# Optimization experiments

Hardware: AMD Instinct MI355X
Metric: run time of the kernel (lower is better)

Reference implementation:

```python
import jax, jax.numpy as jnp
import numpy as np
import math

B, T, D, H = 2, 2048, 1024, 16
HD = D // H


def setup_inputs() -> dict:
    key = jax.random.key(0)
    k1, k2, k3 = jax.random.split(key, 3)
    x = jax.random.normal(k1, (B, T, D), dtype=jnp.float32)
    attn_mask = jnp.ones((B, T), dtype=jnp.int32)
    W_qkv = jax.random.normal(k2, (D, 3 * D), dtype=jnp.float32) * (1.0 / math.sqrt(D))
    W_out = jax.random.normal(k3, (D, D), dtype=jnp.float32) * (1.0 / math.sqrt(D))
    return {"x": x, "attn_mask": attn_mask, "W_qkv": W_qkv, "W_out": W_out}


def reference(x, attn_mask, W_qkv, W_out):
    Bx, Tx, Dx = x.shape
    qkv = jnp.einsum("btd,de->bte", x, W_qkv)  # (B,T,3D)
    q, k, v = jnp.split(qkv, 3, axis=-1)
    # (B,T,D) -> (B,H,T,hd)
    q = q.reshape(Bx, Tx, H, HD).transpose(0, 2, 1, 3)
    k = k.reshape(Bx, Tx, H, HD).transpose(0, 2, 1, 3)
    v = v.reshape(Bx, Tx, H, HD).transpose(0, 2, 1, 3)
    scale = 1.0 / math.sqrt(HD)
    scores = jnp.einsum("bhqd,bhkd->bhqk", q, k) * scale  # (B,H,T,T)
    # padding mask over keys: (B,T) -> (B,1,1,T)
    mask = attn_mask[:, None, None, :]
    scores = jnp.where(mask == 0, jnp.float32(-jnp.inf), scores)
    attn = jax.nn.softmax(scores, axis=-1)
    out = jnp.einsum("bhqk,bhkd->bhqd", attn, v)  # (B,H,T,hd)
    out = out.transpose(0, 2, 1, 3).reshape(Bx, Tx, Dx)
    return jnp.einsum("btd,de->bte", out, W_out)
```

## Files before the change

kernel.cpp:

```cpp
#include <hip/hip_runtime.h>

#define B_ 2
#define T_ 2048
#define D_ 1024
#define H_ 16
#define HD_ 64
#define NT_ (B_*T_)

typedef __attribute__((ext_vector_type(8))) short bf16x8;
typedef __attribute__((ext_vector_type(4))) float f32x4;
typedef __attribute__((ext_vector_type(16))) float f32x16;
typedef __attribute__((ext_vector_type(4))) int i32x4;

#define MFMA32(a, b, c) __builtin_amdgcn_mfma_f32_32x32x16_bf16((a), (b), (c), 0, 0, 0)

static __device__ __forceinline__ unsigned short f2bf(float f) {
    union { float f; unsigned u; } v; v.f = f;
    unsigned r = v.u + 0x7fffu + ((v.u >> 16) & 1u);
    return (unsigned short)(r >> 16);
}

static __device__ __forceinline__ float exp2a(float x) {
    float r; asm("v_exp_f32 %0, %1" : "=v"(r) : "v"(x)); return r;
}

static __device__ __forceinline__ unsigned cvt_pk_bf16(float lo, float hi) {
    unsigned r; asm("v_cvt_pk_bf16_f32 %0, %1, %2" : "=v"(r) : "v"(lo), "v"(hi)); return r;
}

static __device__ __forceinline__ void gload_lds16(const unsigned short* g, unsigned short* l) {
    __builtin_amdgcn_global_load_lds(
        (const __attribute__((address_space(1))) unsigned int*)g,
        (__attribute__((address_space(3))) unsigned int*)l, 16, 0, 0);
}

static __device__ __forceinline__ void xcd_swz(int& bx, int& by) {
    int gx = gridDim.x, nwg = gx * gridDim.y;
    int flat = by * gx + bx;
    int cpx = nwg >> 3;
    int swz = (flat & 7) * cpx + (flat >> 3);
    bx = swz % gx; by = swz / gx;
}

__global__ __launch_bounds__(256) void prep_all(
    const float* __restrict__ x, unsigned short* __restrict__ Xb,
    const float* __restrict__ Wqkv, unsigned short* __restrict__ WqkvT,
    const float* __restrict__ Wout, unsigned short* __restrict__ WoutT) {
    __shared__ float tile[32][33];
    int bid = blockIdx.x, tid = threadIdx.x;
    if (bid < 2048) {
        int base = (bid * 256 + tid) * 8;
        f32x4 a = *(const f32x4*)(x + base);
        f32x4 b = *(const f32x4*)(x + base + 4);
        unsigned short o[8];
#pragma unroll
        for (int j = 0; j < 4; ++j) { o[j] = f2bf(a[j]); o[j + 4] = f2bf(b[j]); }
        *(i32x4*)(Xb + base) = *(const i32x4*)o;
        return;
    }
    const float* in; unsigned short* out; int R, C, bx, by;
    if (bid < 5120) {
        int tb = bid - 2048; bx = tb % 96; by = tb / 96;
        in = Wqkv; out = WqkvT; R = 1024; C = 3072;
    } else {
        int tb = bid - 5120; bx = tb & 31; by = tb >> 5;
        in = Wout; out = WoutT; R = 1024; C = 1024;
    }
    int tx = tid & 31, ty = tid >> 5;
    int c0 = bx * 32, r0 = by * 32;
#pragma unroll
    for (int j = 0; j < 32; j += 8)
        tile[ty + j][tx] = in[(size_t)(r0 + ty + j) * C + c0 + tx];
    __syncthreads();
#pragma unroll
    for (int j = 0; j < 32; j += 8)
        out[(size_t)(c0 + ty + j) * R + r0 + tx] = f2bf(tile[tx][ty + j]);
}

template <int EPI>
__global__ __launch_bounds__(256) void gemm_bt(
    const unsigned short* __restrict__ A, const unsigned short* __restrict__ Bt,
    float* __restrict__ C,
    unsigned short* __restrict__ Qo, unsigned short* __restrict__ Ko,
    unsigned short* __restrict__ Vo,
    int M, int N, int K) {
    __shared__ __align__(16) unsigned short As[128 * 64];
    __shared__ __align__(16) unsigned short Bs[128 * 64];
    int tid = threadIdx.x;
    int wv = tid >> 6, lane = tid & 63;
    int wr = wv >> 1, wc = wv & 1;
    int l15 = lane & 15, lg = lane >> 4;
    int bx = blockIdx.x, by = blockIdx.y;
    xcd_swz(bx, by);
    int tm = by * 128, tn = bx * 128;
    f32x4 acc[4][4] = {};

    int lrow = lane >> 3;
    int scol = ((lane & 7) ^ (lrow & 7)) * 8;
    int rsw = l15 & 7;

    for (int kt = 0; kt < K; kt += 64) {
        __syncthreads();
#pragma unroll
        for (int c = 0; c < 4; ++c) {
            int chunk = wv + c * 4;
            gload_lds16(A + (size_t)(tm + chunk * 8 + lrow) * K + kt + scol, As + chunk * 512);
            gload_lds16(Bt + (size_t)(tn + chunk * 8 + lrow) * K + kt + scol, Bs + chunk * 512);
        }
        __syncthreads();
#pragma unroll
        for (int kk = 0; kk < 2; ++kk) {
            bf16x8 af[4], bfr[4];
#pragma unroll
            for (int m = 0; m < 4; ++m) {
                int row = wr * 64 + m * 16 + l15;
                af[m] = *(const bf16x8*)(As + row * 64 + (((kk * 4 + lg) ^ rsw) * 8));
            }
#pragma unroll
            for (int n = 0; n < 4; ++n) {
                int row = wc * 64 + n * 16 + l15;
                bfr[n] = *(const bf16x8*)(Bs + row * 64 + (((kk * 4 + lg) ^ rsw) * 8));
            }
#pragma unroll
            for (int m = 0; m < 4; ++m)
#pragma unroll
                for (int n = 0; n < 4; ++n)
                    acc[m][n] = __builtin_amdgcn_mfma_f32_16x16x32_bf16(af[m], bfr[n], acc[m][n], 0, 0, 0);
        }
    }

    if (EPI == 0) {
#pragma unroll
        for (int m = 0; m < 4; ++m) {
            int row0 = tm + wr * 64 + m * 16 + lg * 4;
#pragma unroll
            for (int n = 0; n < 4; ++n) {
                int col = tn + wc * 64 + n * 16 + l15;
#pragma unroll
                for (int r = 0; r < 4; ++r)
                    C[(size_t)(row0 + r) * N + col] = acc[m][n][r];
            }
        }
    } else {
        const float SC = 0.125f * 1.44269504f;
#pragma unroll
        for (int m = 0; m < 4; ++m) {
            int row0 = tm + wr * 64 + m * 16 + lg * 4;
#pragma unroll
            for (int n = 0; n < 4; ++n) {
                int e = tn + wc * 64 + n * 16 + l15;
                int sec = e >> 10, rem = e & 1023;
                int h = rem >> 6, hd = rem & 63;
                int tok = row0;
                int b = tok >> 11, tl = tok & 2047;
                if (sec == 2) {
                    size_t idx0 = ((size_t)(b * H_ + h) * HD_ + hd) * T_ + tl;
                    *(unsigned*)(Vo + idx0)     = cvt_pk_bf16(acc[m][n][0], acc[m][n][1]);
                    *(unsigned*)(Vo + idx0 + 2) = cvt_pk_bf16(acc[m][n][2], acc[m][n][3]);
                } else {
                    unsigned short* dst = (sec == 0) ? Qo : Ko;
                    float sc = (sec == 0) ? SC : 1.0f;
#pragma unroll
                    for (int r = 0; r < 4; ++r)
                        dst[(((size_t)(b * H_ + h) * T_ + tl + r) << 6) + hd] =
                            f2bf(acc[m][n][r] * sc);
                }
            }
        }
    }
}

__global__ __launch_bounds__(256) void gemm_n64(
    const unsigned short* __restrict__ A, const unsigned short* __restrict__ Bt,
    float* __restrict__ C, int M, int N, int K) {
    __shared__ __align__(16) unsigned short As[128 * 64];
    __shared__ __align__(16) unsigned short Bs[64 * 64];
    int tid = threadIdx.x;
    int wv = tid >> 6, lane = tid & 63;
    int wr = wv >> 1, wc = wv & 1;
    int l15 = lane & 15, lg = lane >> 4;
    int bx = blockIdx.x, by = blockIdx.y;
    xcd_swz(bx, by);
    int tm = by * 128, tn = bx * 64;
    f32x4 acc[4][2] = {};

    int lrow = lane >> 3;
    int scol = ((lane & 7) ^ (lrow & 7)) * 8;
    int rsw = l15 & 7;

    for (int kt = 0; kt < K; kt += 64) {
        __syncthreads();
#pragma unroll
        for (int c = 0; c < 4; ++c) {
            int chunk = wv + c * 4;
            gload_lds16(A + (size_t)(tm + chunk * 8 + lrow) * K + kt + scol, As + chunk * 512);
        }
#pragma unroll
        for (int c = 0; c < 2; ++c) {
            int chunk = wv + c * 4;
            gload_lds16(Bt + (size_t)(tn + chunk * 8 + lrow) * K + kt + scol, Bs + chunk * 512);
        }
        __syncthreads();
#pragma unroll
        for (int kk = 0; kk < 2; ++kk) {
            bf16x8 af[4], bfr[2];
#pragma unroll
            for (int m = 0; m < 4; ++m) {
                int row = wr * 64 + m * 16 + l15;
                af[m] = *(const bf16x8*)(As + row * 64 + (((kk * 4 + lg) ^ rsw) * 8));
            }
#pragma unroll
            for (int n = 0; n < 2; ++n) {
                int row = wc * 32 + n * 16 + l15;
                bfr[n] = *(const bf16x8*)(Bs + row * 64 + (((kk * 4 + lg) ^ rsw) * 8));
            }
#pragma unroll
            for (int m = 0; m < 4; ++m)
#pragma unroll
                for (int n = 0; n < 2; ++n)
                    acc[m][n] = __builtin_amdgcn_mfma_f32_16x16x32_bf16(af[m], bfr[n], acc[m][n], 0, 0, 0);
        }
    }

#pragma unroll
    for (int m = 0; m < 4; ++m) {
        int row0 = tm + wr * 64 + m * 16 + lg * 4;
#pragma unroll
        for (int n = 0; n < 2; ++n) {
            int col = tn + wc * 32 + n * 16 + l15;
#pragma unroll
            for (int r = 0; r < 4; ++r)
                C[(size_t)(row0 + r) * N + col] = acc[m][n][r];
        }
    }
}

#define KPAD 72
#define VPAD 136

#define EXCH(PV, HF, FRAG)                                                     \
  do {                                                                         \
    unsigned uA0 = cvt_pk_bf16(PV[8 * HF + 0], PV[8 * HF + 1]);                \
    unsigned uA1 = cvt_pk_bf16(PV[8 * HF + 2], PV[8 * HF + 3]);                \
    unsigned uB0 = cvt_pk_bf16(PV[8 * HF + 4], PV[8 * HF + 5]);                \
    unsigned uB1 = cvt_pk_bf16(PV[8 * HF + 6], PV[8 * HF + 7]);                \
    unsigned snd0 = hi ? uA0 : uB0, snd1 = hi ? uA1 : uB1;                     \
    unsigned rc0 = (unsigned)__shfl_xor((int)snd0, 32);                        \
    unsigned rc1 = (unsigned)__shfl_xor((int)snd1, 32);                        \
    union { bf16x8 v; unsigned u[4]; } Fx;                                     \
    Fx.u[0] = hi ? rc0 : uA0;                                                  \
    Fx.u[1] = hi ? rc1 : uA1;                                                  \
    Fx.u[2] = hi ? uB0 : rc0;                                                  \
    Fx.u[3] = hi ? uB1 : rc1;                                                  \
    FRAG = Fx.v;                                                               \
  } while (0)

__global__ __launch_bounds__(256) void flash_attn(
    const unsigned short* __restrict__ Qg, const unsigned short* __restrict__ Kg,
    const unsigned short* __restrict__ VTg, const int* __restrict__ mask,
    unsigned short* __restrict__ AO) {
    __shared__ __align__(16) unsigned short Ks[128 * KPAD];
    __shared__ __align__(16) unsigned short VTs[64 * VPAD];
    __shared__ float biasS[128];

    int tid = threadIdx.x, wv = tid >> 6, lane = tid & 63;
    int l31 = lane & 31, hi = lane >> 5;
    int bx = blockIdx.x, by = blockIdx.y;
    xcd_swz(bx, by);
    int bh = by;
    int b = bh >> 4, h = bh & 15;
    int q0 = bx * 128;
    const unsigned short* Qb  = Qg  + (size_t)bh * T_ * HD_;
    const unsigned short* Kb  = Kg  + (size_t)bh * T_ * HD_;
    const unsigned short* VTb = VTg + (size_t)bh * HD_ * T_;

    bf16x8 qf[4];
    {
        const unsigned short* qrow = Qb + (size_t)(q0 + wv * 32 + l31) * HD_;
#pragma unroll
        for (int c = 0; c < 4; ++c)
            qf[c] = *(const bf16x8*)(qrow + c * 16 + hi * 8);
    }

    float lp0 = 0.f, lp1 = 0.f, lp2 = 0.f, lp3 = 0.f;
    f32x16 o0 = {}, o1 = {};

    i32x4 kv[4], vvv[4];
#pragma unroll
    for (int c = 0; c < 4; ++c) {
        int idx = tid + c * 256;
        kv[c]  = *(const i32x4*)(Kb + (size_t)(idx >> 3) * HD_ + (idx & 7) * 8);
        vvv[c] = *(const i32x4*)(VTb + (size_t)(idx >> 4) * T_ + (idx & 15) * 8);
    }
    int mA = mask[b * T_ + lane];
    int mB = mask[b * T_ + 64 + lane];

    for (int kt = 0; kt < T_; kt += 128) {
        bool nomask = __all(mA != 0 && mB != 0);
        __syncthreads();
#pragma unroll
        for (int c = 0; c < 4; ++c) {
            int idx = tid + c * 256;
            *(i32x4*)(Ks + (idx >> 3) * KPAD + (idx & 7) * 8) = kv[c];
            *(i32x4*)(VTs + (idx >> 4) * VPAD + (idx & 15) * 8) = vvv[c];
        }
        if (!nomask && wv == 0) {
            biasS[lane]      = mA ? 0.f : -1e30f;
            biasS[64 + lane] = mB ? 0.f : -1e30f;
        }
        if (kt + 128 < T_) {
#pragma unroll
            for (int c = 0; c < 4; ++c) {
                int idx = tid + c * 256;
                kv[c]  = *(const i32x4*)(Kb + (size_t)(kt + 128 + (idx >> 3)) * HD_ + (idx & 7) * 8);
                vvv[c] = *(const i32x4*)(VTb + (size_t)(idx >> 4) * T_ + kt + 128 + (idx & 15) * 8);
            }
            mA = mask[b * T_ + kt + 128 + lane];
            mB = mask[b * T_ + kt + 192 + lane];
        }
        __syncthreads();

#pragma unroll
        for (int hp = 0; hp < 2; ++hp) {
            f32x16 s0 = {}, s1 = {};
            __builtin_amdgcn_s_setprio(1);
#pragma unroll
            for (int c = 0; c < 4; ++c) {
                bf16x8 ka = *(const bf16x8*)(Ks + ((hp * 2 + 0) * 32 + l31) * KPAD + c * 16 + hi * 8);
                s0 = MFMA32(ka, qf[c], s0);
            }
#pragma unroll
            for (int c = 0; c < 4; ++c) {
                bf16x8 kb2 = *(const bf16x8*)(Ks + ((hp * 2 + 1) * 32 + l31) * KPAD + c * 16 + hi * 8);
                s1 = MFMA32(kb2, qf[c], s1);
            }
            __builtin_amdgcn_s_setprio(0);

            if (!nomask) {
#pragma unroll
                for (int i = 0; i < 16; ++i) {
                    int krow = (i & 3) + 8 * (i >> 2) + 4 * hi;
                    s0[i] += biasS[hp * 64 + krow];
                    s1[i] += biasS[hp * 64 + 32 + krow];
                }
            }
#pragma unroll
            for (int i = 0; i < 16; i += 4) {
                s0[i] = exp2a(s0[i]);     s0[i+1] = exp2a(s0[i+1]);
                s0[i+2] = exp2a(s0[i+2]); s0[i+3] = exp2a(s0[i+3]);
                s1[i] = exp2a(s1[i]);     s1[i+1] = exp2a(s1[i+1]);
                s1[i+2] = exp2a(s1[i+2]); s1[i+3] = exp2a(s1[i+3]);
                lp0 += s0[i]   + s1[i];
                lp1 += s0[i+1] + s1[i+1];
                lp2 += s0[i+2] + s1[i+2];
                lp3 += s0[i+3] + s1[i+3];
            }
            bf16x8 fr0, fr1, fr2, fr3;
            EXCH(s0, 0, fr0);
            EXCH(s0, 1, fr1);
            EXCH(s1, 0, fr2);
            EXCH(s1, 1, fr3);

            __builtin_amdgcn_s_setprio(1);
#pragma unroll
            for (int kc = 0; kc < 4; ++kc) {
                bf16x8 fr = (kc == 0) ? fr0 : (kc == 1) ? fr1 : (kc == 2) ? fr2 : fr3;
                bf16x8 va = *(const bf16x8*)(VTs + l31 * VPAD + hp * 64 + kc * 16 + hi * 8);
                bf16x8 vb = *(const bf16x8*)(VTs + (32 + l31) * VPAD + hp * 64 + kc * 16 + hi * 8);
                o0 = MFMA32(fr, va, o0);
                o1 = MFMA32(fr, vb, o1);
            }
            __builtin_amdgcn_s_setprio(0);
        }
    }

    float l_part = (lp0 + lp1) + (lp2 + lp3);
    l_part += __shfl_xor(l_part, 32);

    size_t rowD = (size_t)(b * T_ + q0 + wv * 32) * D_ + h * 64;
#pragma unroll
    for (int i = 0; i < 16; ++i) {
        int qrow = (i & 3) + 8 * (i >> 2) + 4 * hi;
        float lq = __shfl(l_part, qrow);
        float inv = 1.0f / lq;
        AO[rowD + (size_t)qrow * D_ + l31]      = f2bf(o0[i] * inv);
        AO[rowD + (size_t)qrow * D_ + 32 + l31] = f2bf(o1[i] * inv);
    }
}

extern "C" void kernel_launch(void* const* d_in, const int* in_sizes, int n_in,
                              void* d_out, int out_size, void* d_ws, size_t ws_size,
                              hipStream_t stream) {
    const float* x    = (const float*)d_in[0];
    const int*   mask = (const int*)d_in[1];
    const float* Wqkv = (const float*)d_in[2];
    const float* Wout = (const float*)d_in[3];
    float* out = (float*)d_out;
    char* ws = (char*)d_ws;

    unsigned short* Xb    = (unsigned short*)(ws);
    unsigned short* WqkvT = (unsigned short*)(ws + (size_t)(8u << 20));
    unsigned short* WoutT = (unsigned short*)(ws + (size_t)(14u << 20));
    unsigned short* Qg    = (unsigned short*)(ws + (size_t)(16u << 20));
    unsigned short* Kg    = (unsigned short*)(ws + (size_t)(24u << 20));
    unsigned short* VT    = (unsigned short*)(ws + (size_t)(32u << 20));
    unsigned short* AO    = Xb;

    prep_all<<<6144, 256, 0, stream>>>(x, Xb, Wqkv, WqkvT, Wout, WoutT);
    gemm_bt<1><<<dim3(3072 / 128, 4096 / 128), 256, 0, stream>>>(
        Xb, WqkvT, nullptr, Qg, Kg, VT, NT_, 3 * D_, D_);
    flash_attn<<<dim3(T_ / 128, B_ * H_), 256, 0, stream>>>(Qg, Kg, VT, mask, AO);
    gemm_n64<<<dim3(1024 / 64, 4096 / 128), 256, 0, stream>>>(
        AO, WoutT, out, NT_, D_, D_);
}
```

Before: 127.7 us.

## Load K/V fragments directly from global memory, dropping LDS staging and barriers

The flash attention kernel no longer stages K and V^T tiles through shared memory with register prefetch and two __syncthreads per tile. Each wave now loads its MFMA K and V fragments straight from global memory (relying on L2/cache reuse across the 4 waves), and reads the mask directly for the bias. This removes LDS writes and reads and block barriers, but every wave re-fetches the same K/V data from global memory and the loads are no longer software-prefetched, so latency is exposed.

```diff
diff --git a/kernel.cpp b/kernel.cpp
--- a/kernel.cpp
+++ b/kernel.cpp
@@ -235,9 +235,6 @@
     }
 }
 
-#define KPAD 72
-#define VPAD 136
-
 #define EXCH(PV, HF, FRAG)                                                     \
   do {                                                                         \
     unsigned uA0 = cvt_pk_bf16(PV[8 * HF + 0], PV[8 * HF + 1]);                \
@@ -259,10 +256,6 @@
     const unsigned short* __restrict__ Qg, const unsigned short* __restrict__ Kg,
     const unsigned short* __restrict__ VTg, const int* __restrict__ mask,
     unsigned short* __restrict__ AO) {
-    __shared__ __align__(16) unsigned short Ks[128 * KPAD];
-    __shared__ __align__(16) unsigned short VTs[64 * VPAD];
-    __shared__ float biasS[128];
-
     int tid = threadIdx.x, wv = tid >> 6, lane = tid & 63;
     int l31 = lane & 31, hi = lane >> 5;
     int bx = blockIdx.x, by = blockIdx.y;
@@ -285,63 +278,45 @@
     float lp0 = 0.f, lp1 = 0.f, lp2 = 0.f, lp3 = 0.f;
     f32x16 o0 = {}, o1 = {};
 
-    i32x4 kv[4], vvv[4];
-#pragma unroll
-    for (int c = 0; c < 4; ++c) {
-        int idx = tid + c * 256;
-        kv[c]  = *(const i32x4*)(Kb + (size_t)(idx >> 3) * HD_ + (idx & 7) * 8);
-        vvv[c] = *(const i32x4*)(VTb + (size_t)(idx >> 4) * T_ + (idx & 15) * 8);
-    }
-    int mA = mask[b * T_ + lane];
-    int mB = mask[b * T_ + 64 + lane];
+    const unsigned short* VT0 = VTb + (size_t)l31 * T_;
+    const unsigned short* VT1 = VTb + (size_t)(32 + l31) * T_;
 
     for (int kt = 0; kt < T_; kt += 128) {
+        int mA = mask[b * T_ + kt + lane];
+        int mB = mask[b * T_ + kt + 64 + lane];
         bool nomask = __all(mA != 0 && mB != 0);
-        __syncthreads();
-#pragma unroll
-        for (int c = 0; c < 4; ++c) {
-            int idx = tid + c * 256;
-            *(i32x4*)(Ks + (idx >> 3) * KPAD + (idx & 7) * 8) = kv[c];
-            *(i32x4*)(VTs + (idx >> 4) * VPAD + (idx & 15) * 8) = vvv[c];
-        }
-        if (!nomask && wv == 0) {
-            biasS[lane]      = mA ? 0.f : -1e30f;
-            biasS[64 + lane] = mB ? 0.f : -1e30f;
-        }
-        if (kt + 128 < T_) {
+
+#pragma unroll
+        for (int hp = 0; hp < 2; ++hp) {
+            int kbase = kt + hp * 64;
+            const unsigned short* Kr0 = Kb + (size_t)(kbase + l31) * HD_ + hi * 8;
+            const unsigned short* Kr1 = Kb + (size_t)(kbase + 32 + l31) * HD_ + hi * 8;
+            bf16x8 ka[4], kb2[4], va[4], vb[4];
 #pragma unroll
             for (int c = 0; c < 4; ++c) {
-                int idx = tid + c * 256;
-                kv[c]  = *(const i32x4*)(Kb + (size_t)(kt + 128 + (idx >> 3)) * HD_ + (idx & 7) * 8);
-                vvv[c] = *(const i32x4*)(VTb + (size_t)(idx >> 4) * T_ + kt + 128 + (idx & 15) * 8);
-            }
-            mA = mask[b * T_ + kt + 128 + lane];
-            mB = mask[b * T_ + kt + 192 + lane];
-        }
-        __syncthreads();
-
-#pragma unroll
-        for (int hp = 0; hp < 2; ++hp) {
+                ka[c]  = *(const bf16x8*)(Kr0 + c * 16);
+                kb2[c] = *(const bf16x8*)(Kr1 + c * 16);
+            }
+#pragma unroll
+            for (int kc = 0; kc < 4; ++kc) {
+                va[kc] = *(const bf16x8*)(VT0 + kbase + kc * 16 + hi * 8);
+                vb[kc] = *(const bf16x8*)(VT1 + kbase + kc * 16 + hi * 8);
+            }
+
             f32x16 s0 = {}, s1 = {};
             __builtin_amdgcn_s_setprio(1);
 #pragma unroll
-            for (int c = 0; c < 4; ++c) {
-                bf16x8 ka = *(const bf16x8*)(Ks + ((hp * 2 + 0) * 32 + l31) * KPAD + c * 16 + hi * 8);
-                s0 = MFMA32(ka, qf[c], s0);
-            }
-#pragma unroll
-            for (int c = 0; c < 4; ++c) {
-                bf16x8 kb2 = *(const bf16x8*)(Ks + ((hp * 2 + 1) * 32 + l31) * KPAD + c * 16 + hi * 8);
-                s1 = MFMA32(kb2, qf[c], s1);
-            }
+            for (int c = 0; c < 4; ++c) s0 = MFMA32(ka[c], qf[c], s0);
+#pragma unroll
+            for (int c = 0; c < 4; ++c) s1 = MFMA32(kb2[c], qf[c], s1);
             __builtin_amdgcn_s_setprio(0);
 
             if (!nomask) {
 #pragma unroll
                 for (int i = 0; i < 16; ++i) {
                     int krow = (i & 3) + 8 * (i >> 2) + 4 * hi;
-                    s0[i] += biasS[hp * 64 + krow];
-                    s1[i] += biasS[hp * 64 + 32 + krow];
+                    s0[i] += (mask[b * T_ + kbase + krow] != 0) ? 0.f : -1e30f;
+                    s1[i] += (mask[b * T_ + kbase + 32 + krow] != 0) ? 0.f : -1e30f;
                 }
             }
 #pragma unroll
@@ -365,10 +340,8 @@
 #pragma unroll
             for (int kc = 0; kc < 4; ++kc) {
                 bf16x8 fr = (kc == 0) ? fr0 : (kc == 1) ? fr1 : (kc == 2) ? fr2 : fr3;
-                bf16x8 va = *(const bf16x8*)(VTs + l31 * VPAD + hp * 64 + kc * 16 + hi * 8);
-                bf16x8 vb = *(const bf16x8*)(VTs + (32 + l31) * VPAD + hp * 64 + kc * 16 + hi * 8);
-                o0 = MFMA32(fr, va, o0);
-                o1 = MFMA32(fr, vb, o1);
+                o0 = MFMA32(fr, va[kc], o0);
+                o1 = MFMA32(fr, vb[kc], o1);
             }
             __builtin_amdgcn_s_setprio(0);
         }
```

New measurement: 194.0 us. 52.0% more time.

## Fuse fp32-to-bf16 conversion of x into QKV GEMM operand loading

Applied to the files above, without the earlier changes.

Removes the separate pass that converts x to bf16 in the prep kernel. The QKV GEMM now loads fp32 x into registers one k-tile ahead, converts it to bf16 and writes it into swizzled LDS. This cuts a full read and write of the activation tensor and shrinks the prep launch. In exchange the GEMM reads twice as many bytes for A and replaces the async global-to-LDS load with register-staged stores, which adds register pressure.

```diff
diff --git a/kernel.cpp b/kernel.cpp
--- a/kernel.cpp
+++ b/kernel.cpp
@@ -43,27 +43,16 @@
 }
 
 __global__ __launch_bounds__(256) void prep_all(
-    const float* __restrict__ x, unsigned short* __restrict__ Xb,
     const float* __restrict__ Wqkv, unsigned short* __restrict__ WqkvT,
     const float* __restrict__ Wout, unsigned short* __restrict__ WoutT) {
     __shared__ float tile[32][33];
     int bid = blockIdx.x, tid = threadIdx.x;
-    if (bid < 2048) {
-        int base = (bid * 256 + tid) * 8;
-        f32x4 a = *(const f32x4*)(x + base);
-        f32x4 b = *(const f32x4*)(x + base + 4);
-        unsigned short o[8];
-#pragma unroll
-        for (int j = 0; j < 4; ++j) { o[j] = f2bf(a[j]); o[j + 4] = f2bf(b[j]); }
-        *(i32x4*)(Xb + base) = *(const i32x4*)o;
-        return;
-    }
     const float* in; unsigned short* out; int R, C, bx, by;
-    if (bid < 5120) {
-        int tb = bid - 2048; bx = tb % 96; by = tb / 96;
+    if (bid < 3072) {
+        bx = bid % 96; by = bid / 96;
         in = Wqkv; out = WqkvT; R = 1024; C = 3072;
     } else {
-        int tb = bid - 5120; bx = tb & 31; by = tb >> 5;
+        int tb = bid - 3072; bx = tb & 31; by = tb >> 5;
         in = Wout; out = WoutT; R = 1024; C = 1024;
     }
     int tx = tid & 31, ty = tid >> 5;
@@ -77,10 +66,8 @@
         out[(size_t)(c0 + ty + j) * R + r0 + tx] = f2bf(tile[tx][ty + j]);
 }
 
-template <int EPI>
-__global__ __launch_bounds__(256) void gemm_bt(
-    const unsigned short* __restrict__ A, const unsigned short* __restrict__ Bt,
-    float* __restrict__ C,
+__global__ __launch_bounds__(256) void gemm_qkv(
+    const float* __restrict__ X, const unsigned short* __restrict__ Bt,
     unsigned short* __restrict__ Qo, unsigned short* __restrict__ Ko,
     unsigned short* __restrict__ Vo,
     int M, int N, int K) {
@@ -99,13 +86,36 @@
     int scol = ((lane & 7) ^ (lrow & 7)) * 8;
     int rsw = l15 & 7;
 
+    f32x4 apre0[4], apre1[4];
+#pragma unroll
+    for (int c = 0; c < 4; ++c) {
+        int chunk = wv + c * 4;
+        const float* ag = X + (size_t)(tm + chunk * 8 + lrow) * K + scol;
+        apre0[c] = *(const f32x4*)(ag);
+        apre1[c] = *(const f32x4*)(ag + 4);
+    }
+
     for (int kt = 0; kt < K; kt += 64) {
         __syncthreads();
 #pragma unroll
         for (int c = 0; c < 4; ++c) {
             int chunk = wv + c * 4;
-            gload_lds16(A + (size_t)(tm + chunk * 8 + lrow) * K + kt + scol, As + chunk * 512);
+            i32x4 w;
+            w[0] = (int)cvt_pk_bf16(apre0[c][0], apre0[c][1]);
+            w[1] = (int)cvt_pk_bf16(apre0[c][2], apre0[c][3]);
+            w[2] = (int)cvt_pk_bf16(apre1[c][0], apre1[c][1]);
+            w[3] = (int)cvt_pk_bf16(apre1[c][2], apre1[c][3]);
+            *(i32x4*)(As + chunk * 512 + lane * 8) = w;
             gload_lds16(Bt + (size_t)(tn + chunk * 8 + lrow) * K + kt + scol, Bs + chunk * 512);
+        }
+        if (kt + 64 < K) {
+#pragma unroll
+            for (int c = 0; c < 4; ++c) {
+                int chunk = wv + c * 4;
+                const float* ag = X + (size_t)(tm + chunk * 8 + lrow) * K + kt + 64 + scol;
+                apre0[c] = *(const f32x4*)(ag);
+                apre1[c] = *(const f32x4*)(ag + 4);
+            }
         }
         __syncthreads();
 #pragma unroll
@@ -129,42 +139,28 @@
         }
     }
 
-    if (EPI == 0) {
-#pragma unroll
-        for (int m = 0; m < 4; ++m) {
-            int row0 = tm + wr * 64 + m * 16 + lg * 4;
-#pragma unroll
-            for (int n = 0; n < 4; ++n) {
-                int col = tn + wc * 64 + n * 16 + l15;
+    const float SC = 0.125f * 1.44269504f;
+#pragma unroll
+    for (int m = 0; m < 4; ++m) {
+        int row0 = tm + wr * 64 + m * 16 + lg * 4;
+#pragma unroll
+        for (int n = 0; n < 4; ++n) {
+            int e = tn + wc * 64 + n * 16 + l15;
+            int sec = e >> 10, rem = e & 1023;
+            int h = rem >> 6, hd = rem & 63;
+            int tok = row0;
+            int b = tok >> 11, tl = tok & 2047;
+            if (sec == 2) {
+                size_t idx0 = ((size_t)(b * H_ + h) * HD_ + hd) * T_ + tl;
+                *(unsigned*)(Vo + idx0)     = cvt_pk_bf16(acc[m][n][0], acc[m][n][1]);
+                *(unsigned*)(Vo + idx0 + 2) = cvt_pk_bf16(acc[m][n][2], acc[m][n][3]);
+            } else {
+                unsigned short* dst = (sec == 0) ? Qo : Ko;
+                float sc = (sec == 0) ? SC : 1.0f;
 #pragma unroll
                 for (int r = 0; r < 4; ++r)
-                    C[(size_t)(row0 + r) * N + col] = acc[m][n][r];
-            }
-        }
-    } else {
-        const float SC = 0.125f * 1.44269504f;
-#pragma unroll
-        for (int m = 0; m < 4; ++m) {
-            int row0 = tm + wr * 64 + m * 16 + lg * 4;
-#pragma unroll
-            for (int n = 0; n < 4; ++n) {
-                int e = tn + wc * 64 + n * 16 + l15;
-                int sec = e >> 10, rem = e & 1023;
-                int h = rem >> 6, hd = rem & 63;
-                int tok = row0;
-                int b = tok >> 11, tl = tok & 2047;
-                if (sec == 2) {
-                    size_t idx0 = ((size_t)(b * H_ + h) * HD_ + hd) * T_ + tl;
-                    *(unsigned*)(Vo + idx0)     = cvt_pk_bf16(acc[m][n][0], acc[m][n][1]);
-                    *(unsigned*)(Vo + idx0 + 2) = cvt_pk_bf16(acc[m][n][2], acc[m][n][3]);
-                } else {
-                    unsigned short* dst = (sec == 0) ? Qo : Ko;
-                    float sc = (sec == 0) ? SC : 1.0f;
-#pragma unroll
-                    for (int r = 0; r < 4; ++r)
-                        dst[(((size_t)(b * H_ + h) * T_ + tl + r) << 6) + hd] =
-                            f2bf(acc[m][n][r] * sc);
-                }
+                    dst[(((size_t)(b * H_ + h) * T_ + tl + r) << 6) + hd] =
+                        f2bf(acc[m][n][r] * sc);
             }
         }
     }
@@ -398,17 +394,16 @@
     float* out = (float*)d_out;
     char* ws = (char*)d_ws;
 
-    unsigned short* Xb    = (unsigned short*)(ws);
+    unsigned short* AO    = (unsigned short*)(ws);
     unsigned short* WqkvT = (unsigned short*)(ws + (size_t)(8u << 20));
     unsigned short* WoutT = (unsigned short*)(ws + (size_t)(14u << 20));
     unsigned short* Qg    = (unsigned short*)(ws + (size_t)(16u << 20));
     unsigned short* Kg    = (unsigned short*)(ws + (size_t)(24u << 20));
     unsigned short* VT    = (unsigned short*)(ws + (size_t)(32u << 20));
-    unsigned short* AO    = Xb;
-
-    prep_all<<<6144, 256, 0, stream>>>(x, Xb, Wqkv, WqkvT, Wout, WoutT);
-    gemm_bt<1><<<dim3(3072 / 128, 4096 / 128), 256, 0, stream>>>(
-        Xb, WqkvT, nullptr, Qg, Kg, VT, NT_, 3 * D_, D_);
+
+    prep_all<<<4096, 256, 0, stream>>>(Wqkv, WqkvT, Wout, WoutT);
+    gemm_qkv<<<dim3(3072 / 128, 4096 / 128), 256, 0, stream>>>(
+        x, WqkvT, Qg, Kg, VT, NT_, 3 * D_, D_);
     flash_attn<<<dim3(T_ / 128, B_ * H_), 256, 0, stream>>>(Qg, Kg, VT, mask, AO);
     gemm_n64<<<dim3(1024 / 64, 4096 / 128), 256, 0, stream>>>(
         AO, WoutT, out, NT_, D_, D_);
```

Measured after the change: 118.4 us. -7.3%, faster.
